# Kernel optimization log

Hardware: AMD Instinct MI355X
Metric: run time of the kernel (lower is better)

## Reference

```python
import jax, jax.numpy as jnp
import numpy as np

B, T, D, H, O, E = 4, 2048, 1024, 2048, 1024, 8
EPS = 1e-12  # torch F.normalize p=1 eps


def setup_inputs() -> dict:
    key = jax.random.key(0)
    ks = jax.random.split(key, 8)
    s = lambda *dims: 1.0 / np.sqrt(dims[0])
    return {
        "x": jax.random.normal(ks[0], (B, T, D), dtype=jnp.float32),
        "num_experts_chosen": 2,
        "W_gate": jax.random.normal(ks[1], (D, E), dtype=jnp.float32) * s(D),
        "b_gate": jnp.zeros((E,), dtype=jnp.float32),
        "W1": jax.random.normal(ks[2], (E, D, H), dtype=jnp.float32) * s(D),
        "b1": jnp.zeros((E, H), dtype=jnp.float32),
        "W2": jax.random.normal(ks[3], (E, H, O), dtype=jnp.float32) * s(H),
        "b2": jnp.zeros((E, O), dtype=jnp.float32),
    }


def reference(x, num_experts_chosen, W_gate, b_gate, W1, b1, W2, b2):
    # Router: softmax over experts -> [b, t, E]
    gating = jax.nn.softmax(jnp.einsum("btd,de->bte", x, W_gate) + b_gate, axis=-1)

    # Top-k mask (scatter of ones at top-k indices), then L1 renormalize
    _, topk_idx = jax.lax.top_k(gating, num_experts_chosen)  # [b, t, k]
    mask = jax.nn.one_hot(topk_idx, E, dtype=gating.dtype).sum(axis=-2)  # [b, t, E]
    g = gating * mask
    g = g / jnp.maximum(jnp.sum(jnp.abs(g), axis=-1, keepdims=True), EPS)

    # Dense compute of ALL experts (faithful to original), eval-mode dropout = identity
    h = jax.nn.relu(jnp.einsum("btd,edh->bteh", x, W1) + b1)  # [b, t, E, H]
    eo = jnp.einsum("bteh,eho->bteo", h, W2) + b2              # [b, t, E, O]

    # Weighted combine over experts
    return jnp.einsum("bte,bteo->bto", g, eo)
```

## Files before the change

kernel.cpp:

```cpp
#include <hip/hip_runtime.h>
#include <hip/hip_bf16.h>

typedef unsigned short u16;
typedef __attribute__((ext_vector_type(8))) short short8;
typedef __attribute__((ext_vector_type(4))) float floatx4;

#define NB 4
#define NT 2048
#define ND 1024
#define NH 2048
#define NO 1024
#define NE 8
#define NTOK (NB * NT)

#define BM 128
#define BN 128
#define BK 32

__device__ __forceinline__ u16 f2bf(float f) {
  __hip_bfloat16 h = __float2bfloat16(f);
  return *reinterpret_cast<u16*>(&h);
}

__device__ __forceinline__ float bf2f(unsigned u) {
  return __uint_as_float(u << 16);
}

__device__ __forceinline__ void async16(const u16* g, u16* l) {
  __builtin_amdgcn_global_load_lds(
      (const __attribute__((address_space(1))) void*)g,
      (__attribute__((address_space(3))) void*)l, 16, 0, 0);
}

__global__ __launch_bounds__(256) void transpose_cvt(
    const float* __restrict__ in, u16* __restrict__ out, int R, int C) {
  __shared__ float tile[64][65];
  int e = blockIdx.z;
  in  += (size_t)e * R * C;
  out += (size_t)e * R * C;
  int c0 = blockIdx.x * 64, r0 = blockIdx.y * 64;
  int t = threadIdx.x;
#pragma unroll
  for (int i = 0; i < 4; ++i) {
    int idx = t + i * 256;
    int r = idx >> 4, cq = idx & 15;
    float4 v = *(const float4*)&in[(size_t)(r0 + r) * C + c0 + cq * 4];
    tile[r][cq * 4 + 0] = v.x; tile[r][cq * 4 + 1] = v.y;
    tile[r][cq * 4 + 2] = v.z; tile[r][cq * 4 + 3] = v.w;
  }
  __syncthreads();
#pragma unroll
  for (int i = 0; i < 4; ++i) {
    int idx = t + i * 256;
    int c = idx >> 4, rq = idx & 15;
    uint2 p;
    p.x = (unsigned)f2bf(tile[rq * 4 + 0][c]) | ((unsigned)f2bf(tile[rq * 4 + 1][c]) << 16);
    p.y = (unsigned)f2bf(tile[rq * 4 + 2][c]) | ((unsigned)f2bf(tile[rq * 4 + 3][c]) << 16);
    *(uint2*)&out[(size_t)(c0 + c) * R + r0 + rq * 4] = p;
  }
}

__global__ __launch_bounds__(256) void router_kernel(
    const float* __restrict__ x, const float* __restrict__ Wg,
    const float* __restrict__ bg, u16* __restrict__ xbf,
    int* __restrict__ counts, int* __restrict__ entries,
    float* __restrict__ wts) {
  __shared__ int   se0[32], se1[32];
  __shared__ float sw0[32], sw1[32];
  int t = threadIdx.x;
  int tl = t >> 3;
  int l8 = t & 7;
  int tok = blockIdx.x * 32 + tl;

  const float* xrow = x + (size_t)tok * ND;
  u16* xbrow = xbf + (size_t)tok * ND;
  float acc[8] = {};
#pragma unroll 4
  for (int i = 0; i < 32; ++i) {
    int d0 = l8 * 4 + i * 32;
    float4 xv = *(const float4*)&xrow[d0];
    uint2 p;
    p.x = (unsigned)f2bf(xv.x) | ((unsigned)f2bf(xv.y) << 16);
    p.y = (unsigned)f2bf(xv.z) | ((unsigned)f2bf(xv.w) << 16);
    *(uint2*)&xbrow[d0] = p;
    const float* wr = Wg + (size_t)d0 * NE;
#pragma unroll
    for (int j = 0; j < 4; ++j) {
      float xs = (j == 0) ? xv.x : (j == 1) ? xv.y : (j == 2) ? xv.z : xv.w;
      float4 w0 = *(const float4*)&wr[j * NE];
      float4 w1 = *(const float4*)&wr[j * NE + 4];
      acc[0] += xs * w0.x; acc[1] += xs * w0.y;
      acc[2] += xs * w0.z; acc[3] += xs * w0.w;
      acc[4] += xs * w1.x; acc[5] += xs * w1.y;
      acc[6] += xs * w1.z; acc[7] += xs * w1.w;
    }
  }
#pragma unroll
  for (int off = 4; off; off >>= 1)
#pragma unroll
    for (int k = 0; k < 8; ++k) acc[k] += __shfl_down(acc[k], off, 8);

  if (l8 == 0) {
    float best = -1e30f, second = -1e30f;
    int e0 = 0, e1 = 0;
#pragma unroll
    for (int i = 0; i < NE; ++i) {
      float L = acc[i] + bg[i];
      if (L > best) { second = best; e1 = e0; best = L; e0 = i; }
      else if (L > second) { second = L; e1 = i; }
    }
    float p1 = __expf(second - best);
    float inv = 1.f / (1.f + p1);
    se0[tl] = e0; se1[tl] = e1;
    sw0[tl] = inv; sw1[tl] = p1 * inv;
  }
  __syncthreads();

  if (t < NE) {
    int e = t;
    int c = 0;
#pragma unroll
    for (int k = 0; k < 32; ++k) c += (se0[k] == e) + (se1[k] == e);
    int pos = atomicAdd(&counts[e * 32], c);
    int base = blockIdx.x * 32;
    for (int k = 0; k < 32; ++k) {
      if (se0[k] == e) { entries[e * NTOK + pos] = (base + k) * 2;     wts[e * NTOK + pos] = sw0[k]; ++pos; }
      if (se1[k] == e) { entries[e * NTOK + pos] = (base + k) * 2 + 1; wts[e * NTOK + pos] = sw1[k]; ++pos; }
    }
  }
}

__global__ __launch_bounds__(256) void gemm1_kernel(
    const u16* __restrict__ xbf, const u16* __restrict__ w1t,
    const float* __restrict__ b1, const int* __restrict__ counts,
    const int* __restrict__ entries, u16* __restrict__ hbuf) {
  int b = blockIdx.x;
  int e = b & 7;
  int r = b >> 3;
  int m0 = (r >> 4) * BM;
  int n0 = (r & 15) * BN;
  int cnt = counts[e * 32];
  if (m0 >= cnt) return;
  int rem = cnt - m0; if (rem > BM) rem = BM;

  __shared__ u16 As[BM * BK];
  __shared__ u16 Bs[BN * BK];
  __shared__ int ent_s[BM];

  int t = threadIdx.x;
  if (t < BM) ent_s[t] = (t < rem) ? entries[e * NTOK + m0 + t] : entries[e * NTOK];
  __syncthreads();

  int lane = t & 63, wv = t >> 6;
  int rl0 = wv * 32 + (lane >> 2);
  int rl1 = rl0 + 16;
  int pg = (((lane & 3) ^ ((rl0 >> 1) & 3))) * 8;
  const u16* gA0 = xbf + (size_t)(ent_s[rl0] >> 1) * ND + pg;
  const u16* gA1 = xbf + (size_t)(ent_s[rl1] >> 1) * ND + pg;
  const u16* Bbase = w1t + (size_t)e * NH * ND + (size_t)n0 * ND;
  const u16* gB0 = Bbase + (size_t)rl0 * ND + pg;
  const u16* gB1 = Bbase + (size_t)rl1 * ND + pg;
  u16* lA0 = As + (wv * 32) * BK;
  u16* lA1 = As + (wv * 32 + 16) * BK;
  u16* lB0 = Bs + (wv * 32) * BK;
  u16* lB1 = Bs + (wv * 32 + 16) * BK;

  int waveM = (wv >> 1) * 64, waveN = (wv & 1) * 64;
  int rA = lane & 15, quad = lane >> 4;
  int cR = (quad ^ ((rA >> 1) & 3)) * 8;
  const short8* aP[4]; const short8* bP[4];
#pragma unroll
  for (int i = 0; i < 4; ++i) {
    aP[i] = (const short8*)&As[(waveM + i * 16 + rA) * BK + cR];
    bP[i] = (const short8*)&Bs[(waveN + i * 16 + rA) * BK + cR];
  }

  floatx4 acc[4][4] = {};
  for (int k0 = 0; k0 < ND; k0 += BK) {
    async16(gA0 + k0, lA0);
    async16(gA1 + k0, lA1);
    async16(gB0 + k0, lB0);
    async16(gB1 + k0, lB1);
    __syncthreads();
    short8 a[4], bb[4];
#pragma unroll
    for (int i = 0; i < 4; ++i) { a[i] = *aP[i]; bb[i] = *bP[i]; }
#pragma unroll
    for (int i = 0; i < 4; ++i)
#pragma unroll
      for (int j = 0; j < 4; ++j)
        acc[i][j] = __builtin_amdgcn_mfma_f32_16x16x32_bf16(a[i], bb[j], acc[i][j], 0, 0, 0);
    __syncthreads();
  }

#pragma unroll
  for (int i = 0; i < 4; ++i)
#pragma unroll
    for (int rr = 0; rr < 4; ++rr) {
      int lm = waveM + i * 16 + quad * 4 + rr;
      if (lm >= rem) continue;
      int ent = ent_s[lm];
      u16* dst = hbuf + (size_t)ent * NH + n0;
#pragma unroll
      for (int j = 0; j < 4; ++j) {
        int col = waveN + j * 16 + rA;
        float v = acc[i][j][rr] + b1[e * NH + n0 + col];
        dst[col] = f2bf(fmaxf(v, 0.f));
      }
    }
}

__global__ __launch_bounds__(256) void gemm2_kernel(
    const u16* __restrict__ hbuf, const u16* __restrict__ w2t,
    const float* __restrict__ b2, const int* __restrict__ counts,
    const int* __restrict__ entries, const float* __restrict__ wts,
    u16* __restrict__ eo) {
  int b = blockIdx.x;
  int e = b & 7;
  int r = b >> 3;
  int m0 = (r >> 3) * BM;
  int n0 = (r & 7) * BN;
  int cnt = counts[e * 32];
  if (m0 >= cnt) return;
  int rem = cnt - m0; if (rem > BM) rem = BM;

  __shared__ u16 As[BM * BK];
  __shared__ u16 Bs[BN * BK];
  __shared__ int ent_s[BM];
  __shared__ float w_s[BM];

  int t = threadIdx.x;
  if (t < BM) {
    int src = (t < rem) ? (e * NTOK + m0 + t) : (e * NTOK);
    ent_s[t] = entries[src];
    w_s[t] = wts[src];
  }
  __syncthreads();

  int lane = t & 63, wv = t >> 6;
  int rl0 = wv * 32 + (lane >> 2);
  int rl1 = rl0 + 16;
  int pg = (((lane & 3) ^ ((rl0 >> 1) & 3))) * 8;
  const u16* gA0 = hbuf + (size_t)ent_s[rl0] * NH + pg;
  const u16* gA1 = hbuf + (size_t)ent_s[rl1] * NH + pg;
  const u16* Bbase = w2t + (size_t)e * NO * NH + (size_t)n0 * NH;
  const u16* gB0 = Bbase + (size_t)rl0 * NH + pg;
  const u16* gB1 = Bbase + (size_t)rl1 * NH + pg;
  u16* lA0 = As + (wv * 32) * BK;
  u16* lA1 = As + (wv * 32 + 16) * BK;
  u16* lB0 = Bs + (wv * 32) * BK;
  u16* lB1 = Bs + (wv * 32 + 16) * BK;

  int waveM = (wv >> 1) * 64, waveN = (wv & 1) * 64;
  int rA = lane & 15, quad = lane >> 4;
  int cR = (quad ^ ((rA >> 1) & 3)) * 8;
  const short8* aP[4]; const short8* bP[4];
#pragma unroll
  for (int i = 0; i < 4; ++i) {
    aP[i] = (const short8*)&As[(waveM + i * 16 + rA) * BK + cR];
    bP[i] = (const short8*)&Bs[(waveN + i * 16 + rA) * BK + cR];
  }

  floatx4 acc[4][4] = {};
  for (int k0 = 0; k0 < NH; k0 += BK) {
    async16(gA0 + k0, lA0);
    async16(gA1 + k0, lA1);
    async16(gB0 + k0, lB0);
    async16(gB1 + k0, lB1);
    __syncthreads();
    short8 a[4], bb[4];
#pragma unroll
    for (int i = 0; i < 4; ++i) { a[i] = *aP[i]; bb[i] = *bP[i]; }
#pragma unroll
    for (int i = 0; i < 4; ++i)
#pragma unroll
      for (int j = 0; j < 4; ++j)
        acc[i][j] = __builtin_amdgcn_mfma_f32_16x16x32_bf16(a[i], bb[j], acc[i][j], 0, 0, 0);
    __syncthreads();
  }

#pragma unroll
  for (int i = 0; i < 4; ++i)
#pragma unroll
    for (int rr = 0; rr < 4; ++rr) {
      int lm = waveM + i * 16 + quad * 4 + rr;
      if (lm >= rem) continue;
      int ent = ent_s[lm];
      float w = w_s[lm];
      u16* dst = eo + (size_t)ent * NO + n0;
#pragma unroll
      for (int j = 0; j < 4; ++j) {
        int col = waveN + j * 16 + rA;
        float v = (acc[i][j][rr] + b2[e * NO + n0 + col]) * w;
        dst[col] = f2bf(v);
      }
    }
}

__global__ __launch_bounds__(256) void combine_kernel(
    const u16* __restrict__ eo, float* __restrict__ out) {
  size_t idx = (size_t)blockIdx.x * 256 + threadIdx.x;
  size_t tok = idx >> 8;
  int oq = (int)(idx & 255) * 4;
  const u16* p0 = eo + (tok * 2) * NO + oq;
  const u16* p1 = p0 + NO;
  uint2 ua = *(const uint2*)p0;
  uint2 ub = *(const uint2*)p1;
  float4 o;
  o.x = bf2f(ua.x & 0xffff) + bf2f(ub.x & 0xffff);
  o.y = bf2f(ua.x >> 16)    + bf2f(ub.x >> 16);
  o.z = bf2f(ua.y & 0xffff) + bf2f(ub.y & 0xffff);
  o.w = bf2f(ua.y >> 16)    + bf2f(ub.y >> 16);
  *(float4*)&out[tok * NO + oq] = o;
}

extern "C" void kernel_launch(void* const* d_in, const int* in_sizes, int n_in,
                              void* d_out, int out_size, void* d_ws, size_t ws_size,
                              hipStream_t stream) {
  (void)in_sizes; (void)n_in; (void)out_size; (void)ws_size;
  const float* x  = (const float*)d_in[0];
  const float* Wg = (const float*)d_in[2];
  const float* bg = (const float*)d_in[3];
  const float* W1 = (const float*)d_in[4];
  const float* b1 = (const float*)d_in[5];
  const float* W2 = (const float*)d_in[6];
  const float* b2 = (const float*)d_in[7];
  float* out = (float*)d_out;

  char* ws = (char*)d_ws;
  size_t off = 0;
  int*   counts  = (int*)(ws + off);   off += NE * 32 * 4;
  int*   entries = (int*)(ws + off);   off += (size_t)NE * NTOK * 4;
  float* wts     = (float*)(ws + off); off += (size_t)NE * NTOK * 4;
  u16*   xbf     = (u16*)(ws + off);   off += (size_t)NTOK * ND * 2;
  u16*   w1t     = (u16*)(ws + off);   off += (size_t)NE * NH * ND * 2;
  u16*   w2t     = (u16*)(ws + off);   off += (size_t)NE * NO * NH * 2;
  u16*   hbuf    = (u16*)(ws + off);   off += (size_t)NTOK * 2 * NH * 2;
  u16*   eo      = w1t;

  hipMemsetAsync(counts, 0, NE * 32 * 4, stream);

  transpose_cvt<<<dim3(NH / 64, ND / 64, NE), 256, 0, stream>>>(W1, w1t, ND, NH);
  transpose_cvt<<<dim3(NO / 64, NH / 64, NE), 256, 0, stream>>>(W2, w2t, NH, NO);
  router_kernel<<<NTOK / 32, 256, 0, stream>>>(x, Wg, bg, xbf, counts, entries, wts);
  gemm1_kernel<<<NE * (NTOK / BM) * (NH / BN), 256, 0, stream>>>(xbf, w1t, b1, counts, entries, hbuf);
  gemm2_kernel<<<NE * (NTOK / BM) * (NO / BN), 256, 0, stream>>>(hbuf, w2t, b2, counts, entries, wts, eo);
  combine_kernel<<<(NTOK * NO / 4) / 256, 256, 0, stream>>>(eo, out);
}
```

Measured before the change: 437.9 us.

## Fuse weight transposes into router and GEMM1 launches to overlap work

Merges the W1 transpose/convert into the router launch and the W2 transpose/convert into the GEMM1 launch, using extra leading blocks and a shared-memory union. This removes two kernel launches and lets weight conversion run alongside routing and the first expert GEMM, filling idle CUs left by the sparse expert blocks. GEMM LDS fragment pointers are also recomputed from a base address instead of held in pointer arrays, to cut register use. The union raises every kernel's LDS to the 64x65 float tile size, which may lower GEMM occupancy.

```diff
diff --git a/kernel.cpp b/kernel.cpp
--- a/kernel.cpp
+++ b/kernel.cpp
@@ -32,21 +32,24 @@
       (__attribute__((address_space(3))) void*)l, 16, 0, 0);
 }
 
-__global__ __launch_bounds__(256) void transpose_cvt(
-    const float* __restrict__ in, u16* __restrict__ out, int R, int C) {
-  __shared__ float tile[64][65];
-  int e = blockIdx.z;
-  in  += (size_t)e * R * C;
-  out += (size_t)e * R * C;
-  int c0 = blockIdx.x * 64, r0 = blockIdx.y * 64;
-  int t = threadIdx.x;
+union Smem {
+  float tile[64][65];
+  struct { u16 As[BM * BK]; u16 Bs[BN * BK];
+           int ent_s[BM]; float w_s[BM]; } g;
+  struct { int se0[32]; int se1[32];
+           float sw0[32]; float sw1[32]; } r;
+};
+
+__device__ void transpose_tile(const float* __restrict__ in, u16* __restrict__ out,
+                               int R, int C, int r0, int c0,
+                               float (*tile)[65], int t) {
 #pragma unroll
   for (int i = 0; i < 4; ++i) {
     int idx = t + i * 256;
-    int r = idx >> 4, cq = idx & 15;
-    float4 v = *(const float4*)&in[(size_t)(r0 + r) * C + c0 + cq * 4];
-    tile[r][cq * 4 + 0] = v.x; tile[r][cq * 4 + 1] = v.y;
-    tile[r][cq * 4 + 2] = v.z; tile[r][cq * 4 + 3] = v.w;
+    int rr = idx >> 4, cq = idx & 15;
+    float4 v = *(const float4*)&in[(size_t)(r0 + rr) * C + c0 + cq * 4];
+    tile[rr][cq * 4 + 0] = v.x; tile[rr][cq * 4 + 1] = v.y;
+    tile[rr][cq * 4 + 2] = v.z; tile[rr][cq * 4 + 3] = v.w;
   }
   __syncthreads();
 #pragma unroll
@@ -60,17 +63,25 @@
   }
 }
 
-__global__ __launch_bounds__(256) void router_kernel(
+__global__ __launch_bounds__(256) void prep1_kernel(
+    const float* __restrict__ W1, u16* __restrict__ w1t,
     const float* __restrict__ x, const float* __restrict__ Wg,
     const float* __restrict__ bg, u16* __restrict__ xbf,
     int* __restrict__ counts, int* __restrict__ entries,
     float* __restrict__ wts) {
-  __shared__ int   se0[32], se1[32];
-  __shared__ float sw0[32], sw1[32];
+  __shared__ Smem sm;
   int t = threadIdx.x;
+  int b = blockIdx.x;
+  if (b < 4096) {
+    int e = b >> 9, r = b & 511;
+    transpose_tile(W1 + (size_t)e * ND * NH, w1t + (size_t)e * ND * NH,
+                   ND, NH, (r >> 5) * 64, (r & 31) * 64, sm.tile, t);
+    return;
+  }
+  int br = b - 4096;
   int tl = t >> 3;
   int l8 = t & 7;
-  int tok = blockIdx.x * 32 + tl;
+  int tok = br * 32 + tl;
 
   const float* xrow = x + (size_t)tok * ND;
   u16* xbrow = xbf + (size_t)tok * ND;
@@ -111,8 +122,8 @@
     }
     float p1 = __expf(second - best);
     float inv = 1.f / (1.f + p1);
-    se0[tl] = e0; se1[tl] = e1;
-    sw0[tl] = inv; sw1[tl] = p1 * inv;
+    sm.r.se0[tl] = e0; sm.r.se1[tl] = e1;
+    sm.r.sw0[tl] = inv; sm.r.sw1[tl] = p1 * inv;
   }
   __syncthreads();
 
@@ -120,21 +131,31 @@
     int e = t;
     int c = 0;
 #pragma unroll
-    for (int k = 0; k < 32; ++k) c += (se0[k] == e) + (se1[k] == e);
+    for (int k = 0; k < 32; ++k) c += (sm.r.se0[k] == e) + (sm.r.se1[k] == e);
     int pos = atomicAdd(&counts[e * 32], c);
-    int base = blockIdx.x * 32;
+    int base = br * 32;
     for (int k = 0; k < 32; ++k) {
-      if (se0[k] == e) { entries[e * NTOK + pos] = (base + k) * 2;     wts[e * NTOK + pos] = sw0[k]; ++pos; }
-      if (se1[k] == e) { entries[e * NTOK + pos] = (base + k) * 2 + 1; wts[e * NTOK + pos] = sw1[k]; ++pos; }
+      if (sm.r.se0[k] == e) { entries[e * NTOK + pos] = (base + k) * 2;     wts[e * NTOK + pos] = sm.r.sw0[k]; ++pos; }
+      if (sm.r.se1[k] == e) { entries[e * NTOK + pos] = (base + k) * 2 + 1; wts[e * NTOK + pos] = sm.r.sw1[k]; ++pos; }
     }
   }
 }
 
 __global__ __launch_bounds__(256) void gemm1_kernel(
+    const float* __restrict__ W2, u16* __restrict__ w2t,
     const u16* __restrict__ xbf, const u16* __restrict__ w1t,
     const float* __restrict__ b1, const int* __restrict__ counts,
     const int* __restrict__ entries, u16* __restrict__ hbuf) {
-  int b = blockIdx.x;
+  __shared__ Smem sm;
+  int t = threadIdx.x;
+  if (blockIdx.x < 4096) {
+    int bb = blockIdx.x;
+    int e = bb >> 9, r = bb & 511;
+    transpose_tile(W2 + (size_t)e * NH * NO, w2t + (size_t)e * NH * NO,
+                   NH, NO, (r >> 4) * 64, (r & 15) * 64, sm.tile, t);
+    return;
+  }
+  int b = blockIdx.x - 4096;
   int e = b & 7;
   int r = b >> 3;
   int m0 = (r >> 4) * BM;
@@ -143,11 +164,7 @@
   if (m0 >= cnt) return;
   int rem = cnt - m0; if (rem > BM) rem = BM;
 
-  __shared__ u16 As[BM * BK];
-  __shared__ u16 Bs[BN * BK];
-  __shared__ int ent_s[BM];
-
-  int t = threadIdx.x;
+  u16* As = sm.g.As; u16* Bs = sm.g.Bs; int* ent_s = sm.g.ent_s;
   if (t < BM) ent_s[t] = (t < rem) ? entries[e * NTOK + m0 + t] : entries[e * NTOK];
   __syncthreads();
 
@@ -168,12 +185,8 @@
   int waveM = (wv >> 1) * 64, waveN = (wv & 1) * 64;
   int rA = lane & 15, quad = lane >> 4;
   int cR = (quad ^ ((rA >> 1) & 3)) * 8;
-  const short8* aP[4]; const short8* bP[4];
-#pragma unroll
-  for (int i = 0; i < 4; ++i) {
-    aP[i] = (const short8*)&As[(waveM + i * 16 + rA) * BK + cR];
-    bP[i] = (const short8*)&Bs[(waveN + i * 16 + rA) * BK + cR];
-  }
+  const u16* aBase = &As[(waveM + rA) * BK + cR];
+  const u16* bBase = &Bs[(waveN + rA) * BK + cR];
 
   floatx4 acc[4][4] = {};
   for (int k0 = 0; k0 < ND; k0 += BK) {
@@ -184,7 +197,10 @@
     __syncthreads();
     short8 a[4], bb[4];
 #pragma unroll
-    for (int i = 0; i < 4; ++i) { a[i] = *aP[i]; bb[i] = *bP[i]; }
+    for (int i = 0; i < 4; ++i) {
+      a[i]  = *(const short8*)(aBase + i * (16 * BK));
+      bb[i] = *(const short8*)(bBase + i * (16 * BK));
+    }
 #pragma unroll
     for (int i = 0; i < 4; ++i)
 #pragma unroll
@@ -215,6 +231,7 @@
     const float* __restrict__ b2, const int* __restrict__ counts,
     const int* __restrict__ entries, const float* __restrict__ wts,
     u16* __restrict__ eo) {
+  __shared__ Smem sm;
   int b = blockIdx.x;
   int e = b & 7;
   int r = b >> 3;
@@ -224,11 +241,8 @@
   if (m0 >= cnt) return;
   int rem = cnt - m0; if (rem > BM) rem = BM;
 
-  __shared__ u16 As[BM * BK];
-  __shared__ u16 Bs[BN * BK];
-  __shared__ int ent_s[BM];
-  __shared__ float w_s[BM];
-
+  u16* As = sm.g.As; u16* Bs = sm.g.Bs;
+  int* ent_s = sm.g.ent_s; float* w_s = sm.g.w_s;
   int t = threadIdx.x;
   if (t < BM) {
     int src = (t < rem) ? (e * NTOK + m0 + t) : (e * NTOK);
@@ -254,12 +268,8 @@
   int waveM = (wv >> 1) * 64, waveN = (wv & 1) * 64;
   int rA = lane & 15, quad = lane >> 4;
   int cR = (quad ^ ((rA >> 1) & 3)) * 8;
-  const short8* aP[4]; const short8* bP[4];
-#pragma unroll
-  for (int i = 0; i < 4; ++i) {
-    aP[i] = (const short8*)&As[(waveM + i * 16 + rA) * BK + cR];
-    bP[i] = (const short8*)&Bs[(waveN + i * 16 + rA) * BK + cR];
-  }
+  const u16* aBase = &As[(waveM + rA) * BK + cR];
+  const u16* bBase = &Bs[(waveN + rA) * BK + cR];
 
   floatx4 acc[4][4] = {};
   for (int k0 = 0; k0 < NH; k0 += BK) {
@@ -270,7 +280,10 @@
     __syncthreads();
     short8 a[4], bb[4];
 #pragma unroll
-    for (int i = 0; i < 4; ++i) { a[i] = *aP[i]; bb[i] = *bP[i]; }
+    for (int i = 0; i < 4; ++i) {
+      a[i]  = *(const short8*)(aBase + i * (16 * BK));
+      bb[i] = *(const short8*)(bBase + i * (16 * BK));
+    }
 #pragma unroll
     for (int i = 0; i < 4; ++i)
 #pragma unroll
@@ -340,10 +353,11 @@
 
   hipMemsetAsync(counts, 0, NE * 32 * 4, stream);
 
-  transpose_cvt<<<dim3(NH / 64, ND / 64, NE), 256, 0, stream>>>(W1, w1t, ND, NH);
-  transpose_cvt<<<dim3(NO / 64, NH / 64, NE), 256, 0, stream>>>(W2, w2t, NH, NO);
-  router_kernel<<<NTOK / 32, 256, 0, stream>>>(x, Wg, bg, xbf, counts, entries, wts);
-  gemm1_kernel<<<NE * (NTOK / BM) * (NH / BN), 256, 0, stream>>>(xbf, w1t, b1, counts, entries, hbuf);
-  gemm2_kernel<<<NE * (NTOK / BM) * (NO / BN), 256, 0, stream>>>(hbuf, w2t, b2, counts, entries, wts, eo);
+  prep1_kernel<<<4096 + NTOK / 32, 256, 0, stream>>>(
+      W1, w1t, x, Wg, bg, xbf, counts, entries, wts);
+  gemm1_kernel<<<4096 + NE * (NTOK / BM) * (NH / BN), 256, 0, stream>>>(
+      W2, w2t, xbf, w1t, b1, counts, entries, hbuf);
+  gemm2_kernel<<<NE * (NTOK / BM) * (NO / BN), 256, 0, stream>>>(
+      hbuf, w2t, b2, counts, entries, wts, eo);
   combine_kernel<<<(NTOK * NO / 4) / 256, 256, 0, stream>>>(eo, out);
 }
```

Measured after the change: 479.1 us. +9.4%, slower.
